# Performance work log

Measured on AMD Instinct MI355X. Metric: run time of the kernel, lower is better.

The kernel has to match this reference:

```python
import jax, jax.numpy as jnp
import numpy as np

EMBED_DIM = 1024
NUM_HEADS = 16
HEAD_DIM = EMBED_DIM // NUM_HEADS


def setup_inputs() -> dict:
    key = jax.random.key(0)
    ks = jax.random.split(key, 11)
    B, S, D = 4, 2048, EMBED_DIM
    s = 1.0 / np.sqrt(D)
    return {
        "q": jax.random.normal(ks[0], (B, S, D), jnp.float32),
        "k": jax.random.normal(ks[1], (B, S, D), jnp.float32),
        "v": jax.random.normal(ks[2], (B, S, D), jnp.float32),
        "Wq": jax.random.normal(ks[3], (D, D), jnp.float32) * s,
        "bq": jnp.zeros((D,), jnp.float32),
        "Wk": jax.random.normal(ks[4], (D, D), jnp.float32) * s,
        "bk": jnp.zeros((D,), jnp.float32),
        "Wv": jax.random.normal(ks[5], (D, D), jnp.float32) * s,
        "bv": jnp.zeros((D,), jnp.float32),
        "Wo": jax.random.normal(ks[6], (D, D), jnp.float32) * s,
        "bo": jnp.zeros((D,), jnp.float32),
    }


def reference(q, k, v, Wq, bq, Wk, bk, Wv, bv, Wo, bo):
    B, S, D = q.shape
    H, Hd = NUM_HEADS, HEAD_DIM
    # projections, split heads -> [B, H, S, Hd]
    qh = (q @ Wq + bq).reshape(B, S, H, Hd).transpose(0, 2, 1, 3)
    kh = (k @ Wk + bk).reshape(B, S, H, Hd).transpose(0, 2, 1, 3)
    vh = (v @ Wv + bv).reshape(B, S, H, Hd).transpose(0, 2, 1, 3)
    scale = 1.0 / jnp.sqrt(jnp.asarray(Hd, qh.dtype))
    scores = jnp.einsum('bhqd,bhkd->bhqk', qh, kh) * scale  # [B,H,S,S]
    attn = jax.nn.softmax(scores, axis=-1)  # dropout = identity in eval
    out = jnp.einsum('bhqk,bhkd->bhqd', attn, vh)
    out = out.transpose(0, 2, 1, 3).reshape(B, S, D)
    return out @ Wo + bo
```

## Files before the change

### kernel.cpp

```cpp
#include <hip/hip_runtime.h>

typedef __attribute__((ext_vector_type(8))) __bf16 bf16x8;
typedef __attribute__((ext_vector_type(4))) __bf16 bf16x4;
typedef __attribute__((ext_vector_type(4))) float f32x4;
typedef __attribute__((ext_vector_type(16))) float f32x16;
typedef __attribute__((ext_vector_type(4))) unsigned int u32x4;

#define GLDS(g, l) __builtin_amdgcn_global_load_lds( \
    (const __attribute__((address_space(1))) void*)(g), \
    (__attribute__((address_space(3))) void*)(l), 16, 0, 0)

__device__ __forceinline__ unsigned cvtpk_bf16(float lo, float hi) {
    unsigned r;
    asm("v_cvt_pk_bf16_f32 %0, %1, %2" : "=v"(r) : "v"(lo), "v"(hi));
    return r;
}
__device__ __forceinline__ void pl32swap(unsigned& a, unsigned& b) {
    asm("v_permlane32_swap_b32 %0, %1" : "+v"(a), "+v"(b));
}

__global__ __launch_bounds__(256) void wtrans2(const float* __restrict__ W0,
                                               const float* __restrict__ W1,
                                               const float* __restrict__ W2,
                                               const float* __restrict__ W3,
                                               __bf16* __restrict__ O0,
                                               __bf16* __restrict__ O1,
                                               __bf16* __restrict__ O2,
                                               __bf16* __restrict__ O3) {
    const int z = blockIdx.z;
    const float* W = z == 0 ? W0 : z == 1 ? W1 : z == 2 ? W2 : W3;
    __bf16* Wt2 = z == 0 ? O0 : z == 1 ? O1 : z == 2 ? O2 : O3;
    __shared__ float lw[64][65];
    const int kt = blockIdx.y * 64, nt = blockIdx.x * 64;
    const int t = threadIdx.x;
    const int r = t >> 4;
    const int c4 = (t & 15) * 4;
    #pragma unroll
    for (int rr = 0; rr < 64; rr += 16) {
        float4 vv = *(const float4*)&W[(size_t)(kt + r + rr) * 1024 + nt + c4];
        lw[r + rr][c4 + 0] = vv.x; lw[r + rr][c4 + 1] = vv.y;
        lw[r + rr][c4 + 2] = vv.z; lw[r + rr][c4 + 3] = vv.w;
    }
    __syncthreads();
    #pragma unroll
    for (int rr = 0; rr < 64; rr += 16) {
        int n = nt + r + rr;
        bf16x4 ov;
        #pragma unroll
        for (int i = 0; i < 4; i++) ov[i] = (__bf16)lw[c4 + i][r + rr];
        int kg = kt + c4;
        size_t off = (size_t)(n >> 7) * 131072 + (size_t)(kg >> 5) * 4096
                   + (size_t)((kg >> 3) & 3) * 1024 + (size_t)(n & 127) * 8 + (kg & 7);
        *(bf16x4*)&Wt2[off] = ov;
    }
}

__global__ __launch_bounds__(256, 3)
void gemm_f32a(const float* __restrict__ A0, const float* __restrict__ A1,
               const float* __restrict__ A2,
               const __bf16* __restrict__ B0, const __bf16* __restrict__ B1,
               const __bf16* __restrict__ B2,
               const float* __restrict__ bi0, const float* __restrict__ bi1,
               const float* __restrict__ bi2,
               void* __restrict__ C0, void* __restrict__ C1, void* __restrict__ C2) {
    __shared__ __align__(16) __bf16 sA[2 * 4096];
    __shared__ __align__(16) __bf16 sB[3 * 4096];
    const int y = blockIdx.y;
    const float* A    = y == 0 ? A0 : y == 1 ? A1 : A2;
    const __bf16* Bt2 = y == 0 ? B0 : y == 1 ? B1 : B2;
    const float* bias = y == 0 ? bi0 : y == 1 ? bi1 : bi2;
    void* Cout        = y == 0 ? C0 : y == 1 ? C1 : C2;
    const int mode    = y + 1;

    const int t = threadIdx.x, l = t & 63, w = t >> 6;
    const int wr = w >> 1, wc = w & 1;
    const int bid = blockIdx.x, slot = bid >> 3;
    const int ytile = (bid & 7) * 8 + (slot & 7);
    const int xtile = slot >> 3;
    const float* Ag = A + (size_t)(ytile * 128 + (t & 127)) * 1024 + (t >> 7) * 16;
    const __bf16* Bb = Bt2 + (size_t)xtile * 131072;
    char* const aw = (char*)sA + ((t >> 7) * 2) * 2048 + (t & 127) * 16;

    float4 rA0, rA1, rA2, rA3;
#define LOADA(T_) do { \
    const float* p_ = Ag + (T_) * 32; \
    rA0 = *(const float4*)p_;        rA1 = *(const float4*)(p_ + 4); \
    rA2 = *(const float4*)(p_ + 8);  rA3 = *(const float4*)(p_ + 12); \
} while (0)
#define WRITEA(buf_) do { \
    bf16x8 o0_, o1_; \
    o0_[0] = (__bf16)rA0.x; o0_[1] = (__bf16)rA0.y; o0_[2] = (__bf16)rA0.z; o0_[3] = (__bf16)rA0.w; \
    o0_[4] = (__bf16)rA1.x; o0_[5] = (__bf16)rA1.y; o0_[6] = (__bf16)rA1.z; o0_[7] = (__bf16)rA1.w; \
    o1_[0] = (__bf16)rA2.x; o1_[1] = (__bf16)rA2.y; o1_[2] = (__bf16)rA2.z; o1_[3] = (__bf16)rA2.w; \
    o1_[4] = (__bf16)rA3.x; o1_[5] = (__bf16)rA3.y; o1_[6] = (__bf16)rA3.z; o1_[7] = (__bf16)rA3.w; \
    *(bf16x8*)(aw + (buf_) * 8192) = o0_; \
    *(bf16x8*)(aw + (buf_) * 8192 + 2048) = o1_; \
} while (0)
#define GLDSB(T_, buf_) do { \
    GLDS(Bb + (T_) * 4096 + t * 8,        (char*)sB + (buf_) * 8192 + t * 16); \
    GLDS(Bb + (T_) * 4096 + 2048 + t * 8, (char*)sB + (buf_) * 8192 + 4096 + t * 16); \
} while (0)

    f32x4 acc[4][4];
    #pragma unroll
    for (int i = 0; i < 4; i++)
        #pragma unroll
        for (int j = 0; j < 4; j++) acc[i][j] = (f32x4){0.f, 0.f, 0.f, 0.f};

    LOADA(0); GLDSB(0, 0);
    WRITEA(0);
    LOADA(1); GLDSB(1, 1);

    int bcur = 0;
    #pragma unroll 1
    for (int T = 0; T < 32; ++T) {
        if (T <= 30) asm volatile("s_waitcnt vmcnt(6) lgkmcnt(0)" ::: "memory");
        else         asm volatile("s_waitcnt vmcnt(0) lgkmcnt(0)" ::: "memory");
        __builtin_amdgcn_s_barrier();
        __builtin_amdgcn_sched_barrier(0);
        if (T <= 30) WRITEA((T + 1) & 1);
        if (T <= 29) { LOADA(T + 2); GLDSB(T + 2, bcur >= 1 ? bcur - 1 : 2); }
        const char* bA = (const char*)sA + (T & 1) * 8192;
        const char* bB = (const char*)sB + bcur * 8192;
        bf16x8 af[4], bfr[4];
        #pragma unroll
        for (int i = 0; i < 4; i++)
            af[i] = *(const bf16x8*)(bA + (l >> 4) * 2048 + (wr * 64 + i * 16 + (l & 15)) * 16);
        #pragma unroll
        for (int j = 0; j < 4; j++)
            bfr[j] = *(const bf16x8*)(bB + (l >> 4) * 2048 + (wc * 64 + j * 16 + (l & 15)) * 16);
        __builtin_amdgcn_s_setprio(1);
        #pragma unroll
        for (int i = 0; i < 4; i++)
            #pragma unroll
            for (int j = 0; j < 4; j++)
                acc[i][j] = __builtin_amdgcn_mfma_f32_16x16x32_bf16(af[i], bfr[j], acc[i][j], 0, 0, 0);
        __builtin_amdgcn_s_setprio(0);
        bcur = bcur == 2 ? 0 : bcur + 1;
    }
#undef LOADA
#undef WRITEA
#undef GLDSB

    const int m0 = ytile * 128, n0 = xtile * 128;
    #pragma unroll
    for (int j = 0; j < 4; j++) {
        int col = n0 + wc * 64 + j * 16 + (l & 15);
        float bv = bias[col];
        #pragma unroll
        for (int i = 0; i < 4; i++) {
            #pragma unroll
            for (int r = 0; r < 4; r++) {
                int row = m0 + wr * 64 + i * 16 + (l >> 4) * 4 + r;
                float vvv = acc[i][j][r] + bv;
                if (mode == 1) {
                    ((__bf16*)Cout)[(size_t)row * 1024 + col] = (__bf16)(vvv * 0.18033688f);
                } else if (mode == 2) {
                    int b_ = row >> 11, s_ = row & 2047, h_ = col >> 6, hd_ = col & 63;
                    size_t off = ((size_t)(b_ * 16 + h_) * 32 + (s_ >> 6)) * 4096
                               + (size_t)(hd_ >> 3) * 512 + (s_ & 63) * 8 + (hd_ & 7);
                    ((__bf16*)Cout)[off] = (__bf16)vvv;
                } else {
                    int b_ = row >> 11, s_ = row & 2047, h_ = col >> 6, d_ = col & 63;
                    size_t off = ((size_t)(b_ * 16 + h_) * 32 + (s_ >> 6)) * 4096
                               + (size_t)((s_ & 63) >> 3) * 512 + (size_t)d_ * 8 + (s_ & 7);
                    ((__bf16*)Cout)[off] = (__bf16)vvv;
                }
            }
        }
    }
}

__global__ __launch_bounds__(256, 2)
void gemm_tt(const __bf16* __restrict__ At, const __bf16* __restrict__ Bt2,
             const float* __restrict__ bias, float* __restrict__ Cout) {
    __shared__ __align__(16) __bf16 sA[3 * 4096];
    __shared__ __align__(16) __bf16 sB[3 * 4096];
    const int t = threadIdx.x, l = t & 63, w = t >> 6;
    const int wr = w >> 1, wc = w & 1;
    const int bid = blockIdx.x, slot = bid >> 3;
    const int ytile = (bid & 7) * 8 + (slot & 7);
    const int xtile = slot >> 3;
    const __bf16* Ab = At + (size_t)ytile * 131072;
    const __bf16* Bb = Bt2 + (size_t)xtile * 131072;

#define GISSUE(ks_, buf_) do { \
    GLDS(Ab + (ks_) * 4096 + t * 8,        (char*)sA + (buf_) * 8192 + t * 16); \
    GLDS(Ab + (ks_) * 4096 + 2048 + t * 8, (char*)sA + (buf_) * 8192 + 4096 + t * 16); \
    GLDS(Bb + (ks_) * 4096 + t * 8,        (char*)sB + (buf_) * 8192 + t * 16); \
    GLDS(Bb + (ks_) * 4096 + 2048 + t * 8, (char*)sB + (buf_) * 8192 + 4096 + t * 16); \
} while (0)

    f32x4 acc[4][4];
    #pragma unroll
    for (int i = 0; i < 4; i++)
        #pragma unroll
        for (int j = 0; j < 4; j++) acc[i][j] = (f32x4){0.f, 0.f, 0.f, 0.f};

    GISSUE(0, 0);
    GISSUE(1, 1);
    int cur = 0;
    #pragma unroll 1
    for (int ks = 0; ks < 32; ++ks) {
        if (ks < 31) asm volatile("s_waitcnt vmcnt(4)" ::: "memory");
        else         asm volatile("s_waitcnt vmcnt(0)" ::: "memory");
        __builtin_amdgcn_s_barrier();
        __builtin_amdgcn_sched_barrier(0);
        if (ks + 2 < 32) GISSUE(ks + 2, cur >= 1 ? cur - 1 : 2);
        const __bf16* bA = sA + cur * 4096;
        const __bf16* bB = sB + cur * 4096;
        bf16x8 af[4], bfr[4];
        #pragma unroll
        for (int i = 0; i < 4; i++)
            af[i] = *(const bf16x8*)(bA + (l >> 4) * 1024 + (wr * 64 + i * 16 + (l & 15)) * 8);
        #pragma unroll
        for (int j = 0; j < 4; j++)
            bfr[j] = *(const bf16x8*)(bB + (l >> 4) * 1024 + (wc * 64 + j * 16 + (l & 15)) * 8);
        __builtin_amdgcn_s_setprio(1);
        #pragma unroll
        for (int i = 0; i < 4; i++)
            #pragma unroll
            for (int j = 0; j < 4; j++)
                acc[i][j] = __builtin_amdgcn_mfma_f32_16x16x32_bf16(af[i], bfr[j], acc[i][j], 0, 0, 0);
        __builtin_amdgcn_s_setprio(0);
        cur = cur == 2 ? 0 : cur + 1;
    }
#undef GISSUE

    const int m0 = ytile * 128, n0 = xtile * 128;
    #pragma unroll
    for (int j = 0; j < 4; j++) {
        int col = n0 + wc * 64 + j * 16 + (l & 15);
        float bv = bias[col];
        #pragma unroll
        for (int i = 0; i < 4; i++) {
            #pragma unroll
            for (int r = 0; r < 4; r++) {
                int row = m0 + wr * 64 + i * 16 + (l >> 4) * 4 + r;
                Cout[(size_t)row * 1024 + col] = acc[i][j][r] + bv;
            }
        }
    }
}

__global__ __launch_bounds__(256, 2)
void attn_fwd(const __bf16* __restrict__ Qp, const __bf16* __restrict__ Kt,
              const __bf16* __restrict__ Vtt, __bf16* __restrict__ AOt) {
    constexpr int S = 2048, D = 1024;
    __shared__ __align__(16) __bf16 sK[3 * 4096];
    __shared__ __align__(16) __bf16 sV[3 * 4096];
    __shared__ float sL[4][64];
    const int t = threadIdx.x, l = t & 63, w = t >> 6;
    const int c = l & 31, g = l >> 5;
    const int bid = blockIdx.x, slot = bid >> 3;
    const int bh = (slot >> 3) * 8 + (bid & 7);
    const int qb = slot & 7;
    const int b = bh >> 4, h = bh & 15;
    const int q0 = qb * 256;
    const __bf16* Kb = Kt + (size_t)bh * 131072;
    const __bf16* Vb = Vtt + (size_t)bh * 131072;

    bf16x8 qf[2][4];
    #pragma unroll
    for (int qh = 0; qh < 2; qh++) {
        const __bf16* qp = Qp + (size_t)(b * S + q0 + w * 64 + qh * 32 + c) * D + h * 64;
        #pragma unroll
        for (int ks = 0; ks < 4; ks++)
            qf[qh][ks] = *(const bf16x8*)(qp + ks * 16 + g * 8);
    }
    asm volatile("s_waitcnt vmcnt(0)" ::: "memory");

#define AISSUE(ti_, buf_) do { \
    GLDS(Kb + (ti_) * 4096 + t * 8,        (char*)sK + (buf_) * 8192 + t * 16); \
    GLDS(Kb + (ti_) * 4096 + 2048 + t * 8, (char*)sK + (buf_) * 8192 + 4096 + t * 16); \
    GLDS(Vb + (ti_) * 4096 + t * 8,        (char*)sV + (buf_) * 8192 + t * 16); \
    GLDS(Vb + (ti_) * 4096 + 2048 + t * 8, (char*)sV + (buf_) * 8192 + 4096 + t * 16); \
} while (0)

    f32x16 acc[2][2];
    acc[0][0] = (f32x16){}; acc[0][1] = (f32x16){};
    acc[1][0] = (f32x16){}; acc[1][1] = (f32x16){};
    float ls[2] = {0.f, 0.f};

    AISSUE(0, 0);
    AISSUE(1, 1);
    int cur = 0;
    #pragma unroll 1
    for (int tile = 0; tile < 32; ++tile) {
        if (tile < 31) asm volatile("s_waitcnt vmcnt(4)" ::: "memory");
        else           asm volatile("s_waitcnt vmcnt(0)" ::: "memory");
        __builtin_amdgcn_s_barrier();
        __builtin_amdgcn_sched_barrier(0);
        const __bf16* bK = sK + cur * 4096;
        const __bf16* bV = sV + cur * 4096;
        #pragma unroll
        for (int kt = 0; kt < 2; kt++) {
            bf16x8 kf[4];
            #pragma unroll
            for (int ks = 0; ks < 4; ks++)
                kf[ks] = *(const bf16x8*)(bK + ((2 * ks + g) * 64 + kt * 32 + c) * 8);
            bf16x8 vq0[2], vq1[2];
            #pragma unroll
            for (int ti = 0; ti < 2; ti++) {
                vq0[ti] = *(const bf16x8*)(bV + ((4 * kt + g) * 64 + ti * 32 + c) * 8);
                vq1[ti] = *(const bf16x8*)(bV + ((4 * kt + 2 + g) * 64 + ti * 32 + c) * 8);
            }
            #pragma unroll
            for (int qh = 0; qh < 2; qh++) {
                f32x16 St = {};
                St = __builtin_amdgcn_mfma_f32_32x32x16_bf16(kf[0], qf[qh][0], St, 0, 0, 0);
                St = __builtin_amdgcn_mfma_f32_32x32x16_bf16(kf[1], qf[qh][1], St, 0, 0, 0);
                St = __builtin_amdgcn_mfma_f32_32x32x16_bf16(kf[2], qf[qh][2], St, 0, 0, 0);
                St = __builtin_amdgcn_mfma_f32_32x32x16_bf16(kf[3], qf[qh][3], St, 0, 0, 0);
                #pragma unroll
                for (int r2 = 0; r2 < 16; r2++) {
                    float p = __builtin_amdgcn_exp2f(St[r2]);
                    ls[qh] += p;
                    St[r2] = p;
                }
                unsigned w0 = cvtpk_bf16(St[0], St[1]),   w1 = cvtpk_bf16(St[2], St[3]);
                unsigned w2 = cvtpk_bf16(St[4], St[5]),   w3 = cvtpk_bf16(St[6], St[7]);
                unsigned w4 = cvtpk_bf16(St[8], St[9]),   w5 = cvtpk_bf16(St[10], St[11]);
                unsigned w6 = cvtpk_bf16(St[12], St[13]), w7 = cvtpk_bf16(St[14], St[15]);
                pl32swap(w0, w2); pl32swap(w1, w3);
                pl32swap(w4, w6); pl32swap(w5, w7);
                bf16x8 pa0 = __builtin_bit_cast(bf16x8, (u32x4){w0, w1, w2, w3});
                bf16x8 pa1 = __builtin_bit_cast(bf16x8, (u32x4){w4, w5, w6, w7});
                acc[qh][0] = __builtin_amdgcn_mfma_f32_32x32x16_bf16(pa0, vq0[0], acc[qh][0], 0, 0, 0);
                acc[qh][1] = __builtin_amdgcn_mfma_f32_32x32x16_bf16(pa0, vq0[1], acc[qh][1], 0, 0, 0);
                acc[qh][0] = __builtin_amdgcn_mfma_f32_32x32x16_bf16(pa1, vq1[0], acc[qh][0], 0, 0, 0);
                acc[qh][1] = __builtin_amdgcn_mfma_f32_32x32x16_bf16(pa1, vq1[1], acc[qh][1], 0, 0, 0);
            }
        }
        if (tile + 2 < 32) AISSUE(tile + 2, cur >= 1 ? cur - 1 : 2);
        cur = cur == 2 ? 0 : cur + 1;
    }
#undef AISSUE

    float tt0 = ls[0] + __shfl_xor(ls[0], 32);
    float tt1 = ls[1] + __shfl_xor(ls[1], 32);
    if (l < 32) { sL[w][l] = 1.0f / tt0; sL[w][32 + l] = 1.0f / tt1; }
    __syncthreads();

    #pragma unroll
    for (int qh = 0; qh < 2; qh++)
        #pragma unroll
        for (int rq = 0; rq < 4; rq++)
            #pragma unroll
            for (int rr2 = 0; rr2 < 4; rr2++) {
                int reg = rq * 4 + rr2;
                int rloc = rr2 + 8 * rq + 4 * g;
                float rn = sL[w][qh * 32 + rloc];
                int qloc = w * 64 + qh * 32 + rloc;
                int mt = b * 16 + qb * 2 + (qloc >> 7);
                int mr = qloc & 127;
                size_t base = ((size_t)mt * 32 + h * 2) * 4096 + (size_t)(c >> 3) * 1024
                            + (size_t)mr * 8 + (c & 7);
                AOt[base] = (__bf16)(acc[qh][0][reg] * rn);
                AOt[base + 4096] = (__bf16)(acc[qh][1][reg] * rn);
            }
}

extern "C" void kernel_launch(void* const* d_in, const int* in_sizes, int n_in,
                              void* d_out, int out_size, void* d_ws, size_t ws_size,
                              hipStream_t stream) {
    const float* q  = (const float*)d_in[0];
    const float* k  = (const float*)d_in[1];
    const float* v  = (const float*)d_in[2];
    const float* Wq = (const float*)d_in[3];
    const float* bq = (const float*)d_in[4];
    const float* Wk = (const float*)d_in[5];
    const float* bk = (const float*)d_in[6];
    const float* Wv = (const float*)d_in[7];
    const float* bv = (const float*)d_in[8];
    const float* Wo = (const float*)d_in[9];
    const float* bo = (const float*)d_in[10];

    char* ws = (char*)d_ws;
    const size_t MiB = 1024 * 1024;
    __bf16* AOt = (__bf16*)(ws);
    __bf16* W2q = (__bf16*)(ws + 48 * MiB);
    __bf16* W2k = (__bf16*)(ws + 50 * MiB);
    __bf16* W2v = (__bf16*)(ws + 52 * MiB);
    __bf16* W2o = (__bf16*)(ws + 54 * MiB);
    __bf16* Qp  = (__bf16*)(ws + 56 * MiB);
    __bf16* Kt  = (__bf16*)(ws + 72 * MiB);
    __bf16* Vtt = (__bf16*)(ws + 88 * MiB);

    wtrans2<<<dim3(16, 16, 4), 256, 0, stream>>>(Wq, Wk, Wv, Wo, W2q, W2k, W2v, W2o);

    gemm_f32a<<<dim3(512, 3), 256, 0, stream>>>(q, k, v, W2q, W2k, W2v,
                                                bq, bk, bv, Qp, Kt, Vtt);

    attn_fwd<<<512, 256, 0, stream>>>(Qp, Kt, Vtt, AOt);

    gemm_tt<<<512, 256, 0, stream>>>(AOt, W2o, bo, (float*)d_out);
}
```

Measured before the change: 234.5 us.

## Pre-convert QKV activations to tiled bf16 and load them with direct-to-LDS copies

Adds a separate kernel that converts the fp32 q/k/v inputs into bf16 and writes them in the tiled layout the GEMM expects, using a swizzled shared-memory staging buffer. The QKV projection GEMM then fetches both A and B through global_load_lds into triple buffers, instead of loading fp32 into registers and converting inside the main loop. This takes register pressure and conversion work out of the GEMM loop, at the cost of an extra kernel launch and an extra round trip of 48 MiB of bf16 data through memory. Occupancy is lowered to 2 blocks per SM to make room for the larger shared-memory footprint.

```diff
diff --git a/kernel.cpp b/kernel.cpp
--- a/kernel.cpp
+++ b/kernel.cpp
@@ -17,6 +17,41 @@
 }
 __device__ __forceinline__ void pl32swap(unsigned& a, unsigned& b) {
     asm("v_permlane32_swap_b32 %0, %1" : "+v"(a), "+v"(b));
+}
+
+__global__ __launch_bounds__(256) void cvt_tile(const float* __restrict__ q,
+                                                const float* __restrict__ k,
+                                                const float* __restrict__ v,
+                                                __bf16* __restrict__ qo,
+                                                __bf16* __restrict__ ko,
+                                                __bf16* __restrict__ vo) {
+    const float* src = blockIdx.z == 0 ? q : blockIdx.z == 1 ? k : v;
+    __bf16* dst = blockIdx.z == 0 ? qo : blockIdx.z == 1 ? ko : vo;
+    __shared__ __align__(16) __bf16 sb[128 * 64];
+    const int t = threadIdx.x;
+    const int m0 = blockIdx.x * 128, kk0 = blockIdx.y * 64;
+    #pragma unroll
+    for (int i = 0; i < 4; i++) {
+        int cid = i * 256 + t;
+        int r = cid >> 3, cc = cid & 7;
+        const float* p = src + (size_t)(m0 + r) * 1024 + kk0 + cc * 8;
+        float4 a = *(const float4*)p;
+        float4 b2 = *(const float4*)(p + 4);
+        bf16x8 o;
+        o[0] = (__bf16)a.x;  o[1] = (__bf16)a.y;  o[2] = (__bf16)a.z;  o[3] = (__bf16)a.w;
+        o[4] = (__bf16)b2.x; o[5] = (__bf16)b2.y; o[6] = (__bf16)b2.z; o[7] = (__bf16)b2.w;
+        *(bf16x8*)((char*)sb + r * 128 + ((cc ^ (r & 7)) << 4)) = o;
+    }
+    __syncthreads();
+    #pragma unroll
+    for (int i = 0; i < 4; i++) {
+        int cid = i * 256 + t;
+        int ch = cid >> 7, r = cid & 127;
+        bf16x8 o = *(const bf16x8*)((const char*)sb + r * 128 + ((ch ^ (r & 7)) << 4));
+        size_t off = (((size_t)blockIdx.x * 32 + blockIdx.y * 2 + (ch >> 2)) * 4 + (ch & 3)) * 1024
+                   + (size_t)r * 8;
+        *(bf16x8*)(dst + off) = o;
+    }
 }
 
 __global__ __launch_bounds__(256) void wtrans2(const float* __restrict__ W0,
@@ -55,18 +90,18 @@
     }
 }
 
-__global__ __launch_bounds__(256, 3)
-void gemm_f32a(const float* __restrict__ A0, const float* __restrict__ A1,
-               const float* __restrict__ A2,
-               const __bf16* __restrict__ B0, const __bf16* __restrict__ B1,
-               const __bf16* __restrict__ B2,
-               const float* __restrict__ bi0, const float* __restrict__ bi1,
-               const float* __restrict__ bi2,
-               void* __restrict__ C0, void* __restrict__ C1, void* __restrict__ C2) {
-    __shared__ __align__(16) __bf16 sA[2 * 4096];
+__global__ __launch_bounds__(256, 2)
+void gemm_qkv(const __bf16* __restrict__ A0, const __bf16* __restrict__ A1,
+              const __bf16* __restrict__ A2,
+              const __bf16* __restrict__ B0, const __bf16* __restrict__ B1,
+              const __bf16* __restrict__ B2,
+              const float* __restrict__ bi0, const float* __restrict__ bi1,
+              const float* __restrict__ bi2,
+              void* __restrict__ C0, void* __restrict__ C1, void* __restrict__ C2) {
+    __shared__ __align__(16) __bf16 sA[3 * 4096];
     __shared__ __align__(16) __bf16 sB[3 * 4096];
     const int y = blockIdx.y;
-    const float* A    = y == 0 ? A0 : y == 1 ? A1 : A2;
+    const __bf16* At  = y == 0 ? A0 : y == 1 ? A1 : A2;
     const __bf16* Bt2 = y == 0 ? B0 : y == 1 ? B1 : B2;
     const float* bias = y == 0 ? bi0 : y == 1 ? bi1 : bi2;
     void* Cout        = y == 0 ? C0 : y == 1 ? C1 : C2;
@@ -77,29 +112,15 @@
     const int bid = blockIdx.x, slot = bid >> 3;
     const int ytile = (bid & 7) * 8 + (slot & 7);
     const int xtile = slot >> 3;
-    const float* Ag = A + (size_t)(ytile * 128 + (t & 127)) * 1024 + (t >> 7) * 16;
+    const __bf16* Ab = At + (size_t)ytile * 131072;
     const __bf16* Bb = Bt2 + (size_t)xtile * 131072;
-    char* const aw = (char*)sA + ((t >> 7) * 2) * 2048 + (t & 127) * 16;
-
-    float4 rA0, rA1, rA2, rA3;
-#define LOADA(T_) do { \
-    const float* p_ = Ag + (T_) * 32; \
-    rA0 = *(const float4*)p_;        rA1 = *(const float4*)(p_ + 4); \
-    rA2 = *(const float4*)(p_ + 8);  rA3 = *(const float4*)(p_ + 12); \
+
+#define GISSUE(ks_, buf_) do { \
+    GLDS(Ab + (ks_) * 4096 + t * 8,        (char*)sA + (buf_) * 8192 + t * 16); \
+    GLDS(Ab + (ks_) * 4096 + 2048 + t * 8, (char*)sA + (buf_) * 8192 + 4096 + t * 16); \
+    GLDS(Bb + (ks_) * 4096 + t * 8,        (char*)sB + (buf_) * 8192 + t * 16); \
+    GLDS(Bb + (ks_) * 4096 + 2048 + t * 8, (char*)sB + (buf_) * 8192 + 4096 + t * 16); \
 } while (0)
-#define WRITEA(buf_) do { \
-    bf16x8 o0_, o1_; \
-    o0_[0] = (__bf16)rA0.x; o0_[1] = (__bf16)rA0.y; o0_[2] = (__bf16)rA0.z; o0_[3] = (__bf16)rA0.w; \
-    o0_[4] = (__bf16)rA1.x; o0_[5] = (__bf16)rA1.y; o0_[6] = (__bf16)rA1.z; o0_[7] = (__bf16)rA1.w; \
-    o1_[0] = (__bf16)rA2.x; o1_[1] = (__bf16)rA2.y; o1_[2] = (__bf16)rA2.z; o1_[3] = (__bf16)rA2.w; \
-    o1_[4] = (__bf16)rA3.x; o1_[5] = (__bf16)rA3.y; o1_[6] = (__bf16)rA3.z; o1_[7] = (__bf16)rA3.w; \
-    *(bf16x8*)(aw + (buf_) * 8192) = o0_; \
-    *(bf16x8*)(aw + (buf_) * 8192 + 2048) = o1_; \
-} while (0)
-#define GLDSB(T_, buf_) do { \
-    GLDS(Bb + (T_) * 4096 + t * 8,        (char*)sB + (buf_) * 8192 + t * 16); \
-    GLDS(Bb + (T_) * 4096 + 2048 + t * 8, (char*)sB + (buf_) * 8192 + 4096 + t * 16); \
-} while (0)
 
     f32x4 acc[4][4];
     #pragma unroll
@@ -107,28 +128,25 @@
         #pragma unroll
         for (int j = 0; j < 4; j++) acc[i][j] = (f32x4){0.f, 0.f, 0.f, 0.f};
 
-    LOADA(0); GLDSB(0, 0);
-    WRITEA(0);
-    LOADA(1); GLDSB(1, 1);
-
-    int bcur = 0;
+    GISSUE(0, 0);
+    GISSUE(1, 1);
+    int cur = 0;
     #pragma unroll 1
-    for (int T = 0; T < 32; ++T) {
-        if (T <= 30) asm volatile("s_waitcnt vmcnt(6) lgkmcnt(0)" ::: "memory");
-        else         asm volatile("s_waitcnt vmcnt(0) lgkmcnt(0)" ::: "memory");
+    for (int ks = 0; ks < 32; ++ks) {
+        if (ks < 31) asm volatile("s_waitcnt vmcnt(4)" ::: "memory");
+        else         asm volatile("s_waitcnt vmcnt(0)" ::: "memory");
         __builtin_amdgcn_s_barrier();
         __builtin_amdgcn_sched_barrier(0);
-        if (T <= 30) WRITEA((T + 1) & 1);
-        if (T <= 29) { LOADA(T + 2); GLDSB(T + 2, bcur >= 1 ? bcur - 1 : 2); }
-        const char* bA = (const char*)sA + (T & 1) * 8192;
-        const char* bB = (const char*)sB + bcur * 8192;
+        if (ks + 2 < 32) GISSUE(ks + 2, cur >= 1 ? cur - 1 : 2);
+        const __bf16* bA = sA + cur * 4096;
+        const __bf16* bB = sB + cur * 4096;
         bf16x8 af[4], bfr[4];
         #pragma unroll
         for (int i = 0; i < 4; i++)
-            af[i] = *(const bf16x8*)(bA + (l >> 4) * 2048 + (wr * 64 + i * 16 + (l & 15)) * 16);
+            af[i] = *(const bf16x8*)(bA + (l >> 4) * 1024 + (wr * 64 + i * 16 + (l & 15)) * 8);
         #pragma unroll
         for (int j = 0; j < 4; j++)
-            bfr[j] = *(const bf16x8*)(bB + (l >> 4) * 2048 + (wc * 64 + j * 16 + (l & 15)) * 16);
+            bfr[j] = *(const bf16x8*)(bB + (l >> 4) * 1024 + (wc * 64 + j * 16 + (l & 15)) * 8);
         __builtin_amdgcn_s_setprio(1);
         #pragma unroll
         for (int i = 0; i < 4; i++)
@@ -136,11 +154,9 @@
             for (int j = 0; j < 4; j++)
                 acc[i][j] = __builtin_amdgcn_mfma_f32_16x16x32_bf16(af[i], bfr[j], acc[i][j], 0, 0, 0);
         __builtin_amdgcn_s_setprio(0);
-        bcur = bcur == 2 ? 0 : bcur + 1;
-    }
-#undef LOADA
-#undef WRITEA
-#undef GLDSB
+        cur = cur == 2 ? 0 : cur + 1;
+    }
+#undef GISSUE
 
     const int m0 = ytile * 128, n0 = xtile * 128;
     #pragma unroll
@@ -172,8 +188,8 @@
 }
 
 __global__ __launch_bounds__(256, 2)
-void gemm_tt(const __bf16* __restrict__ At, const __bf16* __restrict__ Bt2,
-             const float* __restrict__ bias, float* __restrict__ Cout) {
+void gemm_out(const __bf16* __restrict__ At, const __bf16* __restrict__ Bt2,
+              const float* __restrict__ bias, float* __restrict__ Cout) {
     __shared__ __align__(16) __bf16 sA[3 * 4096];
     __shared__ __align__(16) __bf16 sB[3 * 4096];
     const int t = threadIdx.x, l = t & 63, w = t >> 6;
@@ -378,7 +394,9 @@
 
     char* ws = (char*)d_ws;
     const size_t MiB = 1024 * 1024;
-    __bf16* AOt = (__bf16*)(ws);
+    __bf16* Atq = (__bf16*)(ws);
+    __bf16* Atk = (__bf16*)(ws + 16 * MiB);
+    __bf16* Atv = (__bf16*)(ws + 32 * MiB);
     __bf16* W2q = (__bf16*)(ws + 48 * MiB);
     __bf16* W2k = (__bf16*)(ws + 50 * MiB);
     __bf16* W2v = (__bf16*)(ws + 52 * MiB);
@@ -386,13 +404,16 @@
     __bf16* Qp  = (__bf16*)(ws + 56 * MiB);
     __bf16* Kt  = (__bf16*)(ws + 72 * MiB);
     __bf16* Vtt = (__bf16*)(ws + 88 * MiB);
+    __bf16* AOt = (__bf16*)(ws);
+
+    cvt_tile<<<dim3(64, 16, 3), 256, 0, stream>>>(q, k, v, Atq, Atk, Atv);
 
     wtrans2<<<dim3(16, 16, 4), 256, 0, stream>>>(Wq, Wk, Wv, Wo, W2q, W2k, W2v, W2o);
 
-    gemm_f32a<<<dim3(512, 3), 256, 0, stream>>>(q, k, v, W2q, W2k, W2v,
-                                                bq, bk, bv, Qp, Kt, Vtt);
+    gemm_qkv<<<dim3(512, 3), 256, 0, stream>>>(Atq, Atk, Atv, W2q, W2k, W2v,
+                                               bq, bk, bv, Qp, Kt, Vtt);
 
     attn_fwd<<<512, 256, 0, stream>>>(Qp, Kt, Vtt, AOt);
 
-    gemm_tt<<<512, 256, 0, stream>>>(AOt, W2o, bo, (float*)d_out);
-}
+    gemm_out<<<512, 256, 0, stream>>>(AOt, W2o, bo, (float*)d_out);
+}
```

Result: faster. 194.8 us (-16.9%).
